# Kernel optimization log

Hardware: AMD Instinct MI355X
Metric: run time of the kernel (lower is better)

The kernel has to match this reference:

```python
import jax, jax.numpy as jnp
import numpy as np

B, N, F_IN, E, S, L, ITERS = 1, 3072, 64, 4, 32, 3, 5  # batch, nodes, in-feats, edge types, units, layers, GGNN iters


def _gated_graph(h, edges, wz, wr, wh, uz, ur, uh, bz, br):
    # h: [B,N,S]; edges: [E,N,N] (edges[e,m,n] = edge m->n of type e); w*: [E,S,S]
    def step(h, _):
        # activation = edges.transpose(1,2) @ h  -> per-type aggregation of source-node states
        act = jnp.einsum('emn,bms->bens', edges, h)          # [B,E,N,S]
        z = jax.nn.sigmoid(jnp.einsum('bens,esk->bnk', act, wz) + h @ uz + bz)
        r = jax.nn.sigmoid(jnp.einsum('bens,esk->bnk', act, wr) + h @ ur + br)
        hh = jnp.tanh(jnp.einsum('bens,esk->bnk', act, wh) + (r * h) @ uh)
        return z * h + (1.0 - z) * hh, None
    h, _ = jax.lax.scan(step, h, None, length=ITERS)
    return h


def setup_inputs() -> dict:
    key = jax.random.key(0)
    ks = jax.random.split(key, 20)
    x_padded = jax.random.normal(ks[0], (B, N, F_IN), dtype=jnp.float32)
    x_lengths = jnp.full((B,), N, dtype=jnp.int32)
    # sparse 0/1 adjacency per edge type (graph structure), stored dense as in the original
    edges = (jax.random.uniform(ks[1], (E, N, N)) < 0.005).astype(jnp.float32)
    sd = 1.0 / np.sqrt(S)
    fc_w = jax.random.normal(ks[2], (F_IN, S), jnp.float32) / np.sqrt(F_IN)
    fc_b = jnp.zeros((S,), jnp.float32)
    wz = jax.random.normal(ks[3], (L, E, S, S), jnp.float32) * sd
    wr = jax.random.normal(ks[4], (L, E, S, S), jnp.float32) * sd
    wh = jax.random.normal(ks[5], (L, E, S, S), jnp.float32) * sd
    uz = jax.random.normal(ks[6], (L, S, S), jnp.float32) * sd
    ur = jax.random.normal(ks[7], (L, S, S), jnp.float32) * sd
    uh = jax.random.normal(ks[8], (L, S, S), jnp.float32) * sd
    bz = jnp.zeros((L, S), jnp.float32)
    br = jnp.zeros((L, S), jnp.float32)
    out_w = jax.random.normal(ks[9], (S, 5), jnp.float32) * sd
    out_b = jnp.zeros((5,), jnp.float32)
    return {"x_padded": x_padded, "x_lengths": x_lengths, "edges": edges,
            "fc_w": fc_w, "fc_b": fc_b, "wz": wz, "wr": wr, "wh": wh,
            "uz": uz, "ur": ur, "uh": uh, "bz": bz, "br": br,
            "out_w": out_w, "out_b": out_b}


def reference(x_padded, x_lengths, edges, fc_w, fc_b, wz, wr, wh, uz, ur, uh, bz, br, out_w, out_b):
    h = x_padded @ fc_w + fc_b                              # [B,N,S]
    for l in range(L):                                      # 3 stacked GatedGraph layers
        h = _gated_graph(h, edges, wz[l], wr[l], wh[l], uz[l], ur[l], uh[l], bz[l], br[l])
    y = h[:, 5] @ out_w + out_b                             # node index 5 -> [B,5]
    return jax.nn.log_softmax(y, axis=1)
```

## Files before the change

kernel.cpp:

```cpp
#include <hip/hip_runtime.h>

constexpr int N     = 3072;
constexpr int S     = 32;
constexpr int E     = 4;
constexpr int FIN   = 64;
constexpr int CAP   = 64;
constexpr int NNi   = N * N;
constexpr int DUMMY = N;
constexpr int BLK   = 256;
constexpr int TPB   = 768;
constexpr int NPB   = 12;

__device__ __forceinline__ float rl(float v, int lane) {
    return __int_as_float(__builtin_amdgcn_readlane(__float_as_int(v), lane));
}
__device__ __forceinline__ float fast_sigmoid(float x) {
    x = fminf(fmaxf(x, -30.f), 30.f);
    return 1.f / (1.f + __expf(-x));
}
__device__ __forceinline__ float fast_tanh(float x) {
    x = fminf(fmaxf(x, -15.f), 15.f);
    float e = __expf(2.f * x);
    return (e - 1.f) / (e + 1.f);
}

__device__ __forceinline__ float ld_dev(const float* p) {
    return __hip_atomic_load((float*)p, __ATOMIC_RELAXED, __HIP_MEMORY_SCOPE_AGENT);
}
__device__ __forceinline__ void st_dev(float* p, float v) {
    __hip_atomic_store(p, v, __ATOMIC_RELAXED, __HIP_MEMORY_SCOPE_AGENT);
}

__device__ __forceinline__ bool gbar(int* bar, int ph, int b) {
    __shared__ int ok;
    __syncthreads();
    if (threadIdx.x == 0) {
        int* grp  = bar + (b >> 4) * 16;
        int* root = bar + 256;
        int* go   = bar + 272;
        int old = __hip_atomic_fetch_add(grp, 1, __ATOMIC_RELAXED, __HIP_MEMORY_SCOPE_AGENT);
        if (old + 1 == ph * 16) {
            int old2 = __hip_atomic_fetch_add(root, 1, __ATOMIC_RELAXED, __HIP_MEMORY_SCOPE_AGENT);
            if (old2 + 1 == ph * 16)
                __hip_atomic_store(go, ph, __ATOMIC_RELAXED, __HIP_MEMORY_SCOPE_AGENT);
        }
        int spins = 0, okl = 1;
        while (__hip_atomic_load(go, __ATOMIC_RELAXED, __HIP_MEMORY_SCOPE_AGENT) < ph) {
            __builtin_amdgcn_s_sleep(2);
            if (++spins > 300000) { okl = 0; break; }
        }
        ok = okl;
    }
    __syncthreads();
    return ok != 0;
}

__global__ __launch_bounds__(256) void build_csr(const float* __restrict__ edges,
                                                 int* __restrict__ deg,
                                                 int* __restrict__ csr) {
    int t = blockIdx.x * 256 + threadIdx.x;
    int idx4 = t * 4;
    float4 v = *reinterpret_cast<const float4*>(edges + idx4);
    if (v.x == 0.f && v.y == 0.f && v.z == 0.f && v.w == 0.f) return;
    int e   = idx4 / NNi;
    int rem = idx4 - e * NNi;
    int m   = rem / N;
    int nb  = rem - m * N;
    float w[4] = {v.x, v.y, v.z, v.w};
    int base = e * N + nb;
    #pragma unroll
    for (int j = 0; j < 4; ++j) {
        if (w[j] != 0.f) {
            int slot = base + j;
            int pos = atomicAdd(&deg[slot], 1);
            if (pos < CAP) csr[slot * CAP + pos] = m;
        }
    }
}

struct Params {
    const float *x, *fcw, *fcb;
    const float *wz, *wr, *wh, *uz, *ur, *uh, *bz, *br;
    const float *ow, *ob;
    const int   *deg, *csr;
    int   *bar;
    float *h0, *h1, *out;
};

__global__ __launch_bounds__(TPB, 1) void fused_ggnn(Params p) {
    __shared__ __align__(16) float sW[3 * 4096];
    __shared__ __align__(16) float sU[3 * 1024];
    __shared__ float sB[64];

    const int tid  = threadIdx.x;
    const int b    = blockIdx.x;
    const int wid  = tid >> 6;
    const int lane = tid & 63;
    const int s    = lane & 31;
    const int g    = lane >> 5;
    const int n    = b * NPB + wid;

    if (tid < 32 * NPB) {
        int n0 = b * NPB + (tid >> 5);
        int s0 = tid & 31;
        float acc = p.fcb[s0];
        #pragma unroll 8
        for (int k = 0; k < FIN; ++k)
            acc = fmaf(p.x[n0 * FIN + k], p.fcw[k * S + s0], acc);
        st_dev(&p.h0[n0 * S + s0], acc);
    } else if (b == 0) {
        if (tid < 416)      st_dev(&p.h0[DUMMY * S + (tid - 384)], 0.f);
        else if (tid < 448) st_dev(&p.h1[DUMMY * S + (tid - 416)], 0.f);
    }

    const int slot1 = g * N + n;
    const int slot2 = (g + 2) * N + n;
    const int d1 = min(p.deg[slot1], CAP);
    const int d2 = min(p.deg[slot2], CAP);
    const int* __restrict__ l1 = p.csr + slot1 * CAP;
    const int* __restrict__ l2 = p.csr + slot2 * CAP;
    const int dm = max(d1, d2);

    const float* hp = p.h0;
    float*       hn = p.h1;
    float hlast = 0.f;
    int   phase = 1;

    gbar(p.bar, phase, b); phase++;

    for (int l = 0; l < 3; ++l) {
        __syncthreads();
        {
            float4* dw = (float4*)sW;
            const float4* gz = (const float4*)(p.wz + l * 4096);
            const float4* gr = (const float4*)(p.wr + l * 4096);
            const float4* gh = (const float4*)(p.wh + l * 4096);
            for (int i = tid; i < 1024; i += TPB) {
                dw[i] = gz[i]; dw[1024 + i] = gr[i]; dw[2048 + i] = gh[i];
            }
            float4* du = (float4*)sU;
            const float4* guz = (const float4*)(p.uz + l * 1024);
            const float4* gur = (const float4*)(p.ur + l * 1024);
            const float4* guh = (const float4*)(p.uh + l * 1024);
            if (tid < 256) {
                du[tid] = guz[tid]; du[256 + tid] = gur[tid]; du[512 + tid] = guh[tid];
            }
            if (tid < 64) sB[tid] = (tid < 32) ? p.bz[l * 32 + tid]
                                               : p.br[l * 32 + (tid - 32)];
        }
        __syncthreads();

        for (int it = 0; it < 5; ++it) {
            float acc0 = 0.f, acc1 = 0.f;
            for (int c = 0; c < dm; c += 4) {
                int4 ia = *reinterpret_cast<const int4*>(l1 + c);
                int4 ib = *reinterpret_cast<const int4*>(l2 + c);
                int r0 = (c + 0 < d1) ? ia.x : DUMMY;
                int r1 = (c + 1 < d1) ? ia.y : DUMMY;
                int r2 = (c + 2 < d1) ? ia.z : DUMMY;
                int r3 = (c + 3 < d1) ? ia.w : DUMMY;
                int q0 = (c + 0 < d2) ? ib.x : DUMMY;
                int q1 = (c + 1 < d2) ? ib.y : DUMMY;
                int q2 = (c + 2 < d2) ? ib.z : DUMMY;
                int q3 = (c + 3 < d2) ? ib.w : DUMMY;
                float v0 = ld_dev(hp + r0 * S + s), v1 = ld_dev(hp + r1 * S + s);
                float v2 = ld_dev(hp + r2 * S + s), v3 = ld_dev(hp + r3 * S + s);
                float u0 = ld_dev(hp + q0 * S + s), u1 = ld_dev(hp + q1 * S + s);
                float u2 = ld_dev(hp + q2 * S + s), u3 = ld_dev(hp + q3 * S + s);
                acc0 += (v0 + v1) + (v2 + v3);
                acc1 += (u0 + u1) + (u2 + u3);
            }
            const float hval = ld_dev(hp + n * S + s);

            const float* __restrict__ W1 = g ? (sW + 4096) : sW;
            const float* __restrict__ U1 = g ? (sU + 1024) : sU;
            const float* __restrict__ Wh = sW + 8192;
            float accA = sB[g * 32 + s];
            float accB = 0.f;
            float hA = 0.f, hB = 0.f;
            #pragma unroll
            for (int e = 0; e < E; ++e) {
                const float src = (e < 2) ? acc0 : acc1;
                const float* w1c = W1 + e * 1024 + s;
                const float* whc = Wh + e * 1024 + s;
                #pragma unroll
                for (int k = 0; k < 32; k += 2) {
                    float a0 = rl(src, (e & 1) * 32 + k);
                    float a1 = rl(src, (e & 1) * 32 + k + 1);
                    accA = fmaf(a0, w1c[(k)     * 32], accA);
                    accB = fmaf(a1, w1c[(k + 1) * 32], accB);
                    hA   = fmaf(a0, whc[(k)     * 32], hA);
                    hB   = fmaf(a1, whc[(k + 1) * 32], hB);
                }
            }
            #pragma unroll
            for (int k = 0; k < 32; k += 2) {
                accA = fmaf(rl(hval, k),     U1[(k)     * 32 + s], accA);
                accB = fmaf(rl(hval, k + 1), U1[(k + 1) * 32 + s], accB);
            }
            const float zr  = fast_sigmoid(accA + accB);
            const float r_s = __shfl(zr, 32 + s, 64);
            const float z_s = __shfl(zr, s, 64);
            const float rh  = r_s * hval;
            const float* __restrict__ Uh = sU + 2048;
            #pragma unroll
            for (int k = 0; k < 32; k += 2) {
                hA = fmaf(rl(rh, k),     Uh[(k)     * 32 + s], hA);
                hB = fmaf(rl(rh, k + 1), Uh[(k + 1) * 32 + s], hB);
            }
            const float hh   = fast_tanh(hA + hB);
            const float hnew = fmaf(z_s, hval - hh, hh);
            if (g == 0) st_dev(&hn[n * S + s], hnew);
            hlast = hnew;

            float* t = (float*)hp; hp = hn; hn = t;

            if (l != 2 || it != 4) {
                gbar(p.bar, phase, b); phase++;
            }
        }
    }

    if (b == 0 && wid == 5) {
        float y[5];
        #pragma unroll
        for (int j = 0; j < 5; ++j) y[j] = hlast * p.ow[s * 5 + j];
        #pragma unroll
        for (int off = 1; off < 32; off <<= 1) {
            #pragma unroll
            for (int j = 0; j < 5; ++j) y[j] += __shfl_xor(y[j], off, 64);
        }
        #pragma unroll
        for (int j = 0; j < 5; ++j) y[j] += p.ob[j];
        float m = -1e30f;
        #pragma unroll
        for (int j = 0; j < 5; ++j) m = fmaxf(m, y[j]);
        float ssum = 0.f;
        #pragma unroll
        for (int j = 0; j < 5; ++j) ssum += __expf(y[j] - m);
        float lse = m + __logf(ssum);
        #pragma unroll
        for (int j = 0; j < 5; ++j) if (lane == j) p.out[j] = y[j] - lse;
    }
}

__global__ __launch_bounds__(256) void init_h_fb(const float* __restrict__ x,
                                                 const float* __restrict__ fcw,
                                                 const float* __restrict__ fcb,
                                                 float* __restrict__ h0) {
    int t = blockIdx.x * 256 + threadIdx.x;
    int s = t & 31;
    int n = t >> 5;
    float acc = fcb[s];
    #pragma unroll 8
    for (int k = 0; k < FIN; ++k)
        acc = fmaf(x[n * FIN + k], fcw[k * S + s], acc);
    h0[n * S + s] = acc;
}

__global__ __launch_bounds__(512) void ggnn_iter_fb(
    const float* __restrict__ hprev, float* __restrict__ hnext,
    const int* __restrict__ deg, const int* __restrict__ csr,
    const float* __restrict__ wz, const float* __restrict__ wr, const float* __restrict__ wh,
    const float* __restrict__ uz, const float* __restrict__ ur, const float* __restrict__ uh,
    const float* __restrict__ bz, const float* __restrict__ br) {
    __shared__ __align__(16) float sWz[4096];
    __shared__ __align__(16) float sWr[4096];
    __shared__ __align__(16) float sWh[4096];
    __shared__ __align__(16) float sUz[1024], sUr[1024], sUh[1024];

    int tid = threadIdx.x;
    {
        float4*       dz = (float4*)sWz; const float4* gz = (const float4*)wz;
        float4*       dr = (float4*)sWr; const float4* gr = (const float4*)wr;
        float4*       dh = (float4*)sWh; const float4* gh = (const float4*)wh;
        for (int i = tid; i < 1024; i += 512) { dz[i] = gz[i]; dr[i] = gr[i]; dh[i] = gh[i]; }
        float4*       duz = (float4*)sUz; const float4* guz = (const float4*)uz;
        float4*       dur = (float4*)sUr; const float4* gur = (const float4*)ur;
        float4*       duh = (float4*)sUh; const float4* guh = (const float4*)uh;
        if (tid < 256) { duz[tid] = guz[tid]; dur[tid] = gur[tid]; duh[tid] = guh[tid]; }
    }
    __syncthreads();

    const int wid  = tid >> 6;
    const int lane = tid & 63;
    const int s    = lane & 31;
    const int g    = lane >> 5;
    const int n    = blockIdx.x * 8 + wid;

    const int d1 = min(deg[g * N + n], CAP);
    const int d2 = min(deg[(g + 2) * N + n], CAP);
    const int* __restrict__ l1 = csr + (g * N + n) * CAP;
    const int* __restrict__ l2 = csr + ((g + 2) * N + n) * CAP;
    float acc0 = 0.f, acc1 = 0.f;
    const int dmax = max(d1, d2);
    for (int i = 0; i < dmax; ++i) {
        if (i < d1) acc0 += hprev[l1[i] * S + s];
        if (i < d2) acc1 += hprev[l2[i] * S + s];
    }
    const float hval = hprev[n * S + s];

    const float* __restrict__ W1 = g ? sWr : sWz;
    const float* __restrict__ U1 = g ? sUr : sUz;
    float accA = g ? br[s] : bz[s];
    float accB = 0.f;
    float hA = 0.f, hB = 0.f;
    #pragma unroll
    for (int e = 0; e < E; ++e) {
        const float src = (e < 2) ? acc0 : acc1;
        const float* w1c = W1 + e * 1024 + s;
        const float* whc = sWh + e * 1024 + s;
        #pragma unroll
        for (int k = 0; k < 32; k += 2) {
            float a0 = rl(src, (e & 1) * 32 + k);
            float a1 = rl(src, (e & 1) * 32 + k + 1);
            accA = fmaf(a0, w1c[(k)     * 32], accA);
            accB = fmaf(a1, w1c[(k + 1) * 32], accB);
            hA   = fmaf(a0, whc[(k)     * 32], hA);
            hB   = fmaf(a1, whc[(k + 1) * 32], hB);
        }
    }
    #pragma unroll
    for (int k = 0; k < 32; k += 2) {
        accA = fmaf(rl(hval, k),     U1[(k)     * 32 + s], accA);
        accB = fmaf(rl(hval, k + 1), U1[(k + 1) * 32 + s], accB);
    }
    const float zr  = fast_sigmoid(accA + accB);
    const float r_s = __shfl(zr, 32 + s, 64);
    const float z_s = __shfl(zr, s, 64);
    const float rh  = r_s * hval;
    #pragma unroll
    for (int k = 0; k < 32; k += 2) {
        hA = fmaf(rl(rh, k),     sUh[(k)     * 32 + s], hA);
        hB = fmaf(rl(rh, k + 1), sUh[(k + 1) * 32 + s], hB);
    }
    const float hh = fast_tanh(hA + hB);
    const float hnew = fmaf(z_s, hval - hh, hh);
    if (g == 0) hnext[n * S + s] = hnew;
}

__global__ void epilogue_fb(const float* __restrict__ h,
                            const float* __restrict__ ow, const float* __restrict__ ob,
                            float* __restrict__ out) {
    int lane = threadIdx.x;
    float y = 0.f;
    if (lane < 5) {
        y = ob[lane];
        for (int k = 0; k < 32; ++k)
            y = fmaf(h[5 * S + k], ow[k * 5 + lane], y);
    }
    float m = -1e30f;
    #pragma unroll
    for (int j = 0; j < 5; ++j) m = fmaxf(m, __shfl(y, j, 64));
    float ssum = 0.f;
    #pragma unroll
    for (int j = 0; j < 5; ++j) ssum += __expf(__shfl(y, j, 64) - m);
    float lse = m + __logf(ssum);
    if (lane < 5) out[lane] = y - lse;
}

extern "C" void kernel_launch(void* const* d_in, const int* in_sizes, int n_in,
                              void* d_out, int out_size, void* d_ws, size_t ws_size,
                              hipStream_t stream) {
    const float* x     = (const float*)d_in[0];
    const float* edges = (const float*)d_in[2];
    const float* fcw   = (const float*)d_in[3];
    const float* fcb   = (const float*)d_in[4];
    const float* wz    = (const float*)d_in[5];
    const float* wr    = (const float*)d_in[6];
    const float* wh    = (const float*)d_in[7];
    const float* uz    = (const float*)d_in[8];
    const float* ur    = (const float*)d_in[9];
    const float* uh    = (const float*)d_in[10];
    const float* bz    = (const float*)d_in[11];
    const float* br    = (const float*)d_in[12];
    const float* ow    = (const float*)d_in[13];
    const float* ob    = (const float*)d_in[14];

    char* ws = (char*)d_ws;
    float* h0  = (float*)(ws);
    float* h1  = (float*)(ws + 393600);
    int*   deg = (int*)(ws + 787200);
    int*   bar = (int*)(ws + 836352);
    int*   csr = (int*)(ws + 838400);

    hipMemsetAsync(deg, 0, 49152 + 2048, stream);
    build_csr<<<36864, 256, 0, stream>>>(edges, deg, csr);

    Params p;
    p.x = x; p.fcw = fcw; p.fcb = fcb;
    p.wz = wz; p.wr = wr; p.wh = wh;
    p.uz = uz; p.ur = ur; p.uh = uh;
    p.bz = bz; p.br = br; p.ow = ow; p.ob = ob;
    p.deg = deg; p.csr = csr; p.bar = bar;
    p.h0 = h0; p.h1 = h1; p.out = (float*)d_out;

    void* args[] = { &p };
    hipError_t err = hipLaunchCooperativeKernel((const void*)fused_ggnn,
                                                dim3(BLK), dim3(TPB), args, 0, stream);
    if (err != hipSuccess) {
        init_h_fb<<<384, 256, 0, stream>>>(x, fcw, fcb, h0);
        float* ha = h0;
        float* hb = h1;
        for (int l = 0; l < 3; ++l) {
            for (int it = 0; it < 5; ++it) {
                ggnn_iter_fb<<<384, 512, 0, stream>>>(ha, hb, deg, csr,
                    wz + l * 4096, wr + l * 4096, wh + l * 4096,
                    uz + l * 1024, ur + l * 1024, uh + l * 1024,
                    bz + l * 32, br + l * 32);
                float* t = ha; ha = hb; hb = t;
            }
        }
        epilogue_fb<<<1, 64, 0, stream>>>(ha, ow, ob, (float*)d_out);
    }
}
```

Measured before the change: 464.1 us.

## Pack weights for float2 FMAs, keep h in registers, grid-stride CSR build

Weights are repacked into shared memory as interleaved k-pairs so the GRU matvecs can use two-wide vector FMAs (packed FP32 on CDNA). The node's own hidden state now stays in a register across iterations instead of being reloaded from global memory each step. The CSR build becomes a grid-stride loop over 256 blocks instead of 36864 blocks. Launch bounds are loosened and the barrier's failure flag is dropped. Together these aim to cut FMA instruction count, global loads and launch overhead, at the cost of a strided shared-memory repack per layer and fewer threads streaming the large edge tensor.

```diff
diff --git a/kernel.cpp b/kernel.cpp
--- a/kernel.cpp
+++ b/kernel.cpp
@@ -11,6 +11,16 @@
 constexpr int TPB   = 768;
 constexpr int NPB   = 12;
 
+typedef float vfloat2 __attribute__((ext_vector_type(2)));
+
+__device__ __forceinline__ vfloat2 vfma2(vfloat2 a, vfloat2 b, vfloat2 c) {
+#if __has_builtin(__builtin_elementwise_fma)
+    return __builtin_elementwise_fma(a, b, c);
+#else
+    vfloat2 r; r.x = fmaf(a.x, b.x, c.x); r.y = fmaf(a.y, b.y, c.y); return r;
+#endif
+}
+
 __device__ __forceinline__ float rl(float v, int lane) {
     return __int_as_float(__builtin_amdgcn_readlane(__float_as_int(v), lane));
 }
@@ -31,8 +41,7 @@
     __hip_atomic_store(p, v, __ATOMIC_RELAXED, __HIP_MEMORY_SCOPE_AGENT);
 }
 
-__device__ __forceinline__ bool gbar(int* bar, int ph, int b) {
-    __shared__ int ok;
+__device__ __forceinline__ void gbar(int* bar, int ph, int b) {
     __syncthreads();
     if (threadIdx.x == 0) {
         int* grp  = bar + (b >> 4) * 16;
@@ -44,36 +53,36 @@
             if (old2 + 1 == ph * 16)
                 __hip_atomic_store(go, ph, __ATOMIC_RELAXED, __HIP_MEMORY_SCOPE_AGENT);
         }
-        int spins = 0, okl = 1;
+        int spins = 0;
         while (__hip_atomic_load(go, __ATOMIC_RELAXED, __HIP_MEMORY_SCOPE_AGENT) < ph) {
             __builtin_amdgcn_s_sleep(2);
-            if (++spins > 300000) { okl = 0; break; }
-        }
-        ok = okl;
+            if (++spins > 300000) break;
+        }
     }
     __syncthreads();
-    return ok != 0;
 }
 
 __global__ __launch_bounds__(256) void build_csr(const float* __restrict__ edges,
                                                  int* __restrict__ deg,
                                                  int* __restrict__ csr) {
-    int t = blockIdx.x * 256 + threadIdx.x;
-    int idx4 = t * 4;
-    float4 v = *reinterpret_cast<const float4*>(edges + idx4);
-    if (v.x == 0.f && v.y == 0.f && v.z == 0.f && v.w == 0.f) return;
-    int e   = idx4 / NNi;
-    int rem = idx4 - e * NNi;
-    int m   = rem / N;
-    int nb  = rem - m * N;
-    float w[4] = {v.x, v.y, v.z, v.w};
-    int base = e * N + nb;
-    #pragma unroll
-    for (int j = 0; j < 4; ++j) {
-        if (w[j] != 0.f) {
-            int slot = base + j;
-            int pos = atomicAdd(&deg[slot], 1);
-            if (pos < CAP) csr[slot * CAP + pos] = m;
+    const float4* e4 = (const float4*)edges;
+    for (int i = blockIdx.x * 256 + threadIdx.x; i < NNi * E / 4; i += 256 * 256) {
+        float4 v = e4[i];
+        if (v.x == 0.f && v.y == 0.f && v.z == 0.f && v.w == 0.f) continue;
+        int idx4 = i * 4;
+        int e   = idx4 / NNi;
+        int rem = idx4 - e * NNi;
+        int m   = rem / N;
+        int nb  = rem - m * N;
+        float w[4] = {v.x, v.y, v.z, v.w};
+        int base = e * N + nb;
+        #pragma unroll
+        for (int j = 0; j < 4; ++j) {
+            if (w[j] != 0.f) {
+                int slot = base + j;
+                int pos = atomicAdd(&deg[slot], 1);
+                if (pos < CAP) csr[slot * CAP + pos] = m;
+            }
         }
     }
 }
@@ -87,7 +96,7 @@
     float *h0, *h1, *out;
 };
 
-__global__ __launch_bounds__(TPB, 1) void fused_ggnn(Params p) {
+__global__ __launch_bounds__(TPB, 3) void fused_ggnn(Params p) {
     __shared__ __align__(16) float sW[3 * 4096];
     __shared__ __align__(16) float sU[3 * 1024];
     __shared__ float sB[64];
@@ -100,17 +109,18 @@
     const int g    = lane >> 5;
     const int n    = b * NPB + wid;
 
-    if (tid < 32 * NPB) {
-        int n0 = b * NPB + (tid >> 5);
-        int s0 = tid & 31;
-        float acc = p.fcb[s0];
+    float hval;
+    {
+        float acc = p.fcb[s];
         #pragma unroll 8
         for (int k = 0; k < FIN; ++k)
-            acc = fmaf(p.x[n0 * FIN + k], p.fcw[k * S + s0], acc);
-        st_dev(&p.h0[n0 * S + s0], acc);
-    } else if (b == 0) {
-        if (tid < 416)      st_dev(&p.h0[DUMMY * S + (tid - 384)], 0.f);
-        else if (tid < 448) st_dev(&p.h1[DUMMY * S + (tid - 416)], 0.f);
+            acc = fmaf(p.x[n * FIN + k], p.fcw[k * S + s], acc);
+        hval = acc;
+        if (g == 0) st_dev(&p.h0[n * S + s], acc);
+    }
+    if (b == 0) {
+        if (tid < 32)      st_dev(&p.h0[DUMMY * S + tid], 0.f);
+        else if (tid < 64) st_dev(&p.h1[DUMMY * S + (tid - 32)], 0.f);
     }
 
     const int slot1 = g * N + n;
@@ -123,27 +133,33 @@
 
     const float* hp = p.h0;
     float*       hn = p.h1;
-    float hlast = 0.f;
-    int   phase = 1;
-
+    int phase = 1;
     gbar(p.bar, phase, b); phase++;
 
     for (int l = 0; l < 3; ++l) {
         __syncthreads();
         {
-            float4* dw = (float4*)sW;
-            const float4* gz = (const float4*)(p.wz + l * 4096);
-            const float4* gr = (const float4*)(p.wr + l * 4096);
-            const float4* gh = (const float4*)(p.wh + l * 4096);
-            for (int i = tid; i < 1024; i += TPB) {
-                dw[i] = gz[i]; dw[1024 + i] = gr[i]; dw[2048 + i] = gh[i];
-            }
-            float4* du = (float4*)sU;
-            const float4* guz = (const float4*)(p.uz + l * 1024);
-            const float4* gur = (const float4*)(p.ur + l * 1024);
-            const float4* guh = (const float4*)(p.uh + l * 1024);
-            if (tid < 256) {
-                du[tid] = guz[tid]; du[256 + tid] = gur[tid]; du[512 + tid] = guh[tid];
+            const float* gsrc[3] = { p.wz + l * 4096, p.wr + l * 4096, p.wh + l * 4096 };
+            for (int j = tid; j < 6144; j += TPB) {
+                int mat = j >> 11;
+                int r   = j & 2047;
+                int e   = r >> 9;
+                int rr  = r & 511;
+                int k2  = rr >> 5;
+                int ss  = rr & 31;
+                const float* src = gsrc[mat] + e * 1024 + (2 * k2) * 32 + ss;
+                float2 val = { src[0], src[32] };
+                *(float2*)(sW + mat * 4096 + e * 1024 + k2 * 64 + ss * 2) = val;
+            }
+            const float* usrc[3] = { p.uz + l * 1024, p.ur + l * 1024, p.uh + l * 1024 };
+            for (int j = tid; j < 1536; j += TPB) {
+                int mat = j >> 9;
+                int rr  = j & 511;
+                int k2  = rr >> 5;
+                int ss  = rr & 31;
+                const float* src = usrc[mat] + (2 * k2) * 32 + ss;
+                float2 val = { src[0], src[32] };
+                *(float2*)(sU + mat * 1024 + k2 * 64 + ss * 2) = val;
             }
             if (tid < 64) sB[tid] = (tid < 32) ? p.bz[l * 32 + tid]
                                                : p.br[l * 32 + (tid - 32)];
@@ -170,50 +186,55 @@
                 acc0 += (v0 + v1) + (v2 + v3);
                 acc1 += (u0 + u1) + (u2 + u3);
             }
-            const float hval = ld_dev(hp + n * S + s);
 
             const float* __restrict__ W1 = g ? (sW + 4096) : sW;
             const float* __restrict__ U1 = g ? (sU + 1024) : sU;
             const float* __restrict__ Wh = sW + 8192;
-            float accA = sB[g * 32 + s];
-            float accB = 0.f;
-            float hA = 0.f, hB = 0.f;
+            vfloat2 gAcc = { sB[g * 32 + s], 0.f };
+            vfloat2 hAcc = { 0.f, 0.f };
             #pragma unroll
             for (int e = 0; e < E; ++e) {
-                const float src = (e < 2) ? acc0 : acc1;
-                const float* w1c = W1 + e * 1024 + s;
-                const float* whc = Wh + e * 1024 + s;
+                const float src  = (e < 2) ? acc0 : acc1;
+                const int   base = (e & 1) * 32;
+                const float* w1c = W1 + e * 1024 + s * 2;
+                const float* whc = Wh + e * 1024 + s * 2;
                 #pragma unroll
-                for (int k = 0; k < 32; k += 2) {
-                    float a0 = rl(src, (e & 1) * 32 + k);
-                    float a1 = rl(src, (e & 1) * 32 + k + 1);
-                    accA = fmaf(a0, w1c[(k)     * 32], accA);
-                    accB = fmaf(a1, w1c[(k + 1) * 32], accB);
-                    hA   = fmaf(a0, whc[(k)     * 32], hA);
-                    hB   = fmaf(a1, whc[(k + 1) * 32], hB);
+                for (int k2 = 0; k2 < 16; ++k2) {
+                    vfloat2 a2 = { rl(src, base + 2 * k2), rl(src, base + 2 * k2 + 1) };
+                    vfloat2 w2 = *(const vfloat2*)(w1c + k2 * 64);
+                    vfloat2 h2 = *(const vfloat2*)(whc + k2 * 64);
+                    gAcc = vfma2(a2, w2, gAcc);
+                    hAcc = vfma2(a2, h2, hAcc);
                 }
             }
-            #pragma unroll
-            for (int k = 0; k < 32; k += 2) {
-                accA = fmaf(rl(hval, k),     U1[(k)     * 32 + s], accA);
-                accB = fmaf(rl(hval, k + 1), U1[(k + 1) * 32 + s], accB);
-            }
-            const float zr  = fast_sigmoid(accA + accB);
+            {
+                const float* u1c = U1 + s * 2;
+                #pragma unroll
+                for (int k2 = 0; k2 < 16; ++k2) {
+                    vfloat2 a2 = { rl(hval, 2 * k2), rl(hval, 2 * k2 + 1) };
+                    vfloat2 u2 = *(const vfloat2*)(u1c + k2 * 64);
+                    gAcc = vfma2(a2, u2, gAcc);
+                }
+            }
+            const float zr  = fast_sigmoid(gAcc.x + gAcc.y);
             const float r_s = __shfl(zr, 32 + s, 64);
             const float z_s = __shfl(zr, s, 64);
             const float rh  = r_s * hval;
-            const float* __restrict__ Uh = sU + 2048;
-            #pragma unroll
-            for (int k = 0; k < 32; k += 2) {
-                hA = fmaf(rl(rh, k),     Uh[(k)     * 32 + s], hA);
-                hB = fmaf(rl(rh, k + 1), Uh[(k + 1) * 32 + s], hB);
-            }
-            const float hh   = fast_tanh(hA + hB);
+            {
+                const float* uhc = sU + 2048 + s * 2;
+                #pragma unroll
+                for (int k2 = 0; k2 < 16; ++k2) {
+                    vfloat2 a2 = { rl(rh, 2 * k2), rl(rh, 2 * k2 + 1) };
+                    vfloat2 u2 = *(const vfloat2*)(uhc + k2 * 64);
+                    hAcc = vfma2(a2, u2, hAcc);
+                }
+            }
+            const float hh   = fast_tanh(hAcc.x + hAcc.y);
             const float hnew = fmaf(z_s, hval - hh, hh);
             if (g == 0) st_dev(&hn[n * S + s], hnew);
-            hlast = hnew;
-
-            float* t = (float*)hp; hp = hn; hn = t;
+            hval = hnew;
+
+            const float* t = hp; hp = hn; hn = (float*)t;
 
             if (l != 2 || it != 4) {
                 gbar(p.bar, phase, b); phase++;
@@ -224,7 +245,7 @@
     if (b == 0 && wid == 5) {
         float y[5];
         #pragma unroll
-        for (int j = 0; j < 5; ++j) y[j] = hlast * p.ow[s * 5 + j];
+        for (int j = 0; j < 5; ++j) y[j] = hval * p.ow[s * 5 + j];
         #pragma unroll
         for (int off = 1; off < 32; off <<= 1) {
             #pragma unroll
@@ -385,7 +406,7 @@
     int*   csr = (int*)(ws + 838400);
 
     hipMemsetAsync(deg, 0, 49152 + 2048, stream);
-    build_csr<<<36864, 256, 0, stream>>>(edges, deg, csr);
+    build_csr<<<256, 256, 0, stream>>>(edges, deg, csr);
 
     Params p;
     p.x = x; p.fcw = fcw; p.fcb = fcb;
```

Result: slower. 582.0 us (+25.4%).
